# Kernel optimization log

Hardware: AMD Instinct MI355X
Metric: run time of the kernel (lower is better)

Reference implementation:

```python
import jax, jax.numpy as jnp
import numpy as np

N = 50000   # nodes
E = 800000  # edges
D = 256     # input feature dim
H = 128     # hidden size
OUT = 40    # output classes


def setup_inputs() -> dict:
    key = jax.random.key(0)
    ks = jax.random.split(key, 10)
    s = 0.05
    return {
        "x": jax.random.normal(ks[0], (N, D), jnp.float32),
        "edge_index": jax.random.randint(ks[1], (2, E), 0, N, dtype=jnp.int64),
        "W0": jax.random.normal(ks[2], (D, H), jnp.float32) * s,
        "b0": jnp.zeros((H,), jnp.float32),
        "W1": jax.random.normal(ks[3], (H, H), jnp.float32) * s,
        "b1": jnp.zeros((H,), jnp.float32),
        "W2": jax.random.normal(ks[4], (H, H), jnp.float32) * s,
        "b2": jnp.zeros((H,), jnp.float32),
        "Wout": jax.random.normal(ks[5], (H * 3, OUT), jnp.float32) * s,
        "bout": jnp.zeros((OUT,), jnp.float32),
    }


def _gcn_norm(edge_index, n):
    # PyG gcn_norm: add self-loops, symmetric D^-1/2 (A+I) D^-1/2 weights
    row, col = edge_index[0], edge_index[1]
    loop = jnp.arange(n, dtype=edge_index.dtype)
    row = jnp.concatenate([row, loop])
    col = jnp.concatenate([col, loop])
    deg = jax.ops.segment_sum(jnp.ones_like(col, jnp.float32), col, num_segments=n)
    dinv = jnp.where(deg > 0, jax.lax.rsqrt(jnp.maximum(deg, 1.0)), 0.0)
    norm = dinv[row] * dinv[col]  # [E+N]
    return row, col, norm


def _gcn_conv(x, W, b, row, col, norm, n):
    h = x @ W                                   # dense transform first (PyG order)
    msg = h[row] * norm[:, None]                # gather source feats, scale
    out = jax.ops.segment_sum(msg, col, num_segments=n)  # scatter-aggregate
    return out + b


def reference(x, edge_index, W0, b0, W1, b1, W2, b2, Wout, bout):
    n = x.shape[0]
    row, col, norm = _gcn_norm(edge_index, n)
    x1 = jax.nn.relu(_gcn_conv(x, W0, b0, row, col, norm, n))
    x2 = jax.nn.relu(_gcn_conv(x1, W1, b1, row, col, norm, n))
    x3 = jax.nn.relu(_gcn_conv(x2, W2, b2, row, col, norm, n))
    xs = jnp.concatenate([x1, x2, x3], axis=-1)  # JumpingKnowledge 'cat'
    return xs @ Wout + bout
```

## Files before the change

kernel.cpp:

```cpp
#include <hip/hip_runtime.h>

#define HID 128
#define NOUT 40
#define SCAN_B 256

typedef __attribute__((ext_vector_type(8))) short bf16x8;
typedef __attribute__((ext_vector_type(4))) float f32x4;

__device__ inline float bf2f(unsigned int u) {
    unsigned int t = u << 16;
    float f;
    __builtin_memcpy(&f, &t, 4);
    return f;
}
__device__ inline unsigned short f2bf(float f) {
    unsigned int x;
    __builtin_memcpy(&x, &f, 4);
    unsigned int r = (x + 0x7fffu + ((x >> 16) & 1u)) >> 16;
    return (unsigned short)r;
}
__device__ inline bf16x8 pack_bf8(float4 u, float4 v) {
    bf16x8 r;
    r[0] = (short)f2bf(u.x); r[1] = (short)f2bf(u.y);
    r[2] = (short)f2bf(u.z); r[3] = (short)f2bf(u.w);
    r[4] = (short)f2bf(v.x); r[5] = (short)f2bf(v.y);
    r[6] = (short)f2bf(v.z); r[7] = (short)f2bf(v.w);
    return r;
}

__global__ void detect_fmt_kernel(const unsigned int* __restrict__ e, int* __restrict__ flag) {
    int t = threadIdx.x;
    unsigned int v = e[2 * t + 1];
    unsigned long long ball = __ballot(v == 0u);
    if (t == 0) *flag = (ball == ~0ull) ? 1 : 0;
}

__global__ void degree_kernel(const void* __restrict__ eix, const int* __restrict__ flag,
                              int* __restrict__ deg, int E) {
    int i = blockIdx.x * blockDim.x + threadIdx.x;
    if (i >= E) return;
    int f = *flag;
    int c = f ? (int)(((const long long*)eix)[(size_t)E + i]) : ((const int*)eix)[(size_t)E + i];
    atomicAdd(&deg[c], 1);
}

__global__ void scan1_kernel(const int* __restrict__ deg, int* __restrict__ offs,
                             int* __restrict__ bsum, float* __restrict__ dinv, int N) {
    __shared__ int s[SCAN_B];
    int i = blockIdx.x * SCAN_B + threadIdx.x;
    int v = (i < N) ? deg[i] : 0;
    if (i < N) dinv[i] = rsqrtf((float)v + 1.0f);
    s[threadIdx.x] = v;
    __syncthreads();
    for (int d = 1; d < SCAN_B; d <<= 1) {
        int t = (threadIdx.x >= d) ? s[threadIdx.x - d] : 0;
        __syncthreads();
        s[threadIdx.x] += t;
        __syncthreads();
    }
    if (i < N) offs[i] = s[threadIdx.x] - v;
    if (threadIdx.x == SCAN_B - 1) bsum[blockIdx.x] = s[SCAN_B - 1];
}

__global__ void scan2_kernel(int* __restrict__ bsum, int nb) {
    __shared__ int s[SCAN_B];
    int v = (threadIdx.x < nb) ? bsum[threadIdx.x] : 0;
    s[threadIdx.x] = v;
    __syncthreads();
    for (int d = 1; d < SCAN_B; d <<= 1) {
        int t = (threadIdx.x >= d) ? s[threadIdx.x - d] : 0;
        __syncthreads();
        s[threadIdx.x] += t;
        __syncthreads();
    }
    if (threadIdx.x < nb) bsum[threadIdx.x] = s[threadIdx.x] - v;
}

__global__ void scan3_kernel(int* __restrict__ offs, const int* __restrict__ bsum,
                             int* __restrict__ cursor, int N, int E) {
    int i = blockIdx.x * SCAN_B + threadIdx.x;
    if (i < N) {
        int v = offs[i] + bsum[blockIdx.x];
        offs[i] = v;
        cursor[i] = v;
    }
    if (blockIdx.x == 0 && threadIdx.x == 0) offs[N] = E;
}

__global__ void fill_csr_kernel(const void* __restrict__ eix, const int* __restrict__ flag,
                                const float* __restrict__ dinv, int* __restrict__ cursor,
                                int2* __restrict__ pkd, int E) {
    int e = blockIdx.x * blockDim.x + threadIdx.x;
    if (e >= E) return;
    int f = *flag;
    int r, c;
    if (f) {
        r = (int)(((const long long*)eix)[e]);
        c = (int)(((const long long*)eix)[(size_t)E + e]);
    } else {
        r = ((const int*)eix)[e];
        c = ((const int*)eix)[(size_t)E + e];
    }
    int p = atomicAdd(&cursor[c], 1);
    float wv = dinv[r] * dinv[c];
    int2 rec;
    rec.x = r;
    rec.y = __float_as_int(wv);
    pkd[p] = rec;
}

__global__ void wt_all_kernel(const float* __restrict__ W0, const float* __restrict__ W1,
                              const float* __restrict__ W2, const float* __restrict__ Wo,
                              unsigned short* __restrict__ W0t, unsigned short* __restrict__ W1t,
                              unsigned short* __restrict__ W2t, unsigned short* __restrict__ Wot) {
    int idx = blockIdx.x * blockDim.x + threadIdx.x;
    const int s0 = 128 * 256, s1 = 128 * 128, s2 = 128 * 128, s3 = 48 * 384;
    if (idx < s0) {
        int n = idx >> 8, k = idx & 255;
        W0t[idx] = f2bf(W0[(size_t)k * 128 + n]);
    } else if ((idx -= s0) < s1) {
        int n = idx >> 7, k = idx & 127;
        W1t[idx] = f2bf(W1[(size_t)k * 128 + n]);
    } else if ((idx -= s1) < s2) {
        int n = idx >> 7, k = idx & 127;
        W2t[idx] = f2bf(W2[(size_t)k * 128 + n]);
    } else if ((idx -= s2) < s3) {
        int n = idx / 384, k = idx - n * 384;
        Wot[idx] = (n < NOUT) ? f2bf(Wo[(size_t)k * NOUT + n]) : (unsigned short)0;
    }
}

template <bool AF32>
__global__ __launch_bounds__(256) void gemm_mfma_kernel(
    const void* __restrict__ Ap, const unsigned short* __restrict__ Wt,
    unsigned short* __restrict__ H, int M, int K) {
    const int tid = threadIdx.x;
    const int lane = tid & 63;
    const int w = tid >> 6;
    const int wr = w >> 1, wc = w & 1;
    const int lr = lane & 15;
    const int ko = lane >> 4;
    const int bm = blockIdx.x * 64;

    f32x4 acc[2][4];
#pragma unroll
    for (int i = 0; i < 2; ++i)
#pragma unroll
        for (int j = 0; j < 4; ++j) acc[i][j] = (f32x4){0.f, 0.f, 0.f, 0.f};

    size_t aoff[2];
#pragma unroll
    for (int mi = 0; mi < 2; ++mi) {
        int R = bm + wr * 32 + mi * 16 + lr;
        if (R >= M) R = M - 1;
        aoff[mi] = (size_t)R * K + ko * 8;
    }
    size_t boff[4];
#pragma unroll
    for (int ni = 0; ni < 4; ++ni) {
        int n = wc * 64 + ni * 16 + lr;
        boff[ni] = (size_t)n * K + ko * 8;
    }

#pragma unroll 4
    for (int k0 = 0; k0 < K; k0 += 32) {
        bf16x8 a[2], b[4];
#pragma unroll
        for (int mi = 0; mi < 2; ++mi) {
            if constexpr (AF32) {
                const float* p = (const float*)Ap + aoff[mi] + k0;
                float4 u = *(const float4*)p;
                float4 v = *(const float4*)(p + 4);
                a[mi] = pack_bf8(u, v);
            } else {
                a[mi] = *(const bf16x8*)((const unsigned short*)Ap + aoff[mi] + k0);
            }
        }
#pragma unroll
        for (int ni = 0; ni < 4; ++ni) b[ni] = *(const bf16x8*)(Wt + boff[ni] + k0);
#pragma unroll
        for (int mi = 0; mi < 2; ++mi)
#pragma unroll
            for (int ni = 0; ni < 4; ++ni)
                acc[mi][ni] = __builtin_amdgcn_mfma_f32_16x16x32_bf16(a[mi], b[ni], acc[mi][ni], 0, 0, 0);
    }

#pragma unroll
    for (int mi = 0; mi < 2; ++mi) {
        int Rb = bm + wr * 32 + mi * 16 + ko * 4;
#pragma unroll
        for (int r = 0; r < 4; ++r) {
            int R = Rb + r;
            if (R < M) {
#pragma unroll
                for (int ni = 0; ni < 4; ++ni) {
                    int C = wc * 64 + ni * 16 + lr;
                    H[(size_t)R * HID + C] = f2bf(acc[mi][ni][r]);
                }
            }
        }
    }
}

__global__ __launch_bounds__(256) void agg_csr_kernel(
    const unsigned int* __restrict__ h32, const int* __restrict__ offs,
    const int2* __restrict__ pkd, const float* __restrict__ dinv,
    const float* __restrict__ bias, unsigned int* __restrict__ xo, int N) {
    const int lane = threadIdx.x & 63;
    const int n = (blockIdx.x * blockDim.x + threadIdx.x) >> 6;
    if (n >= N) return;
    const float d = dinv[n];
    unsigned int sv = h32[(size_t)n * 64 + lane];
    float ax = bf2f(sv & 0xffff) * (d * d) + bias[2 * lane + 0];
    float ay = bf2f(sv >> 16) * (d * d) + bias[2 * lane + 1];
    int e = offs[n];
    const int e1 = offs[n + 1];

    for (; e + 16 <= e1; e += 16) {
        int2 pk[16];
        unsigned int v[16];
#pragma unroll
        for (int j = 0; j < 16; ++j) pk[j] = pkd[e + j];
#pragma unroll
        for (int j = 0; j < 16; ++j) v[j] = h32[(size_t)pk[j].x * 64 + lane];
#pragma unroll
        for (int j = 0; j < 16; ++j) {
            float wv = __int_as_float(pk[j].y);
            ax += bf2f(v[j] & 0xffff) * wv;
            ay += bf2f(v[j] >> 16) * wv;
        }
    }
    for (; e + 4 <= e1; e += 4) {
        int2 pk[4];
        unsigned int v[4];
#pragma unroll
        for (int j = 0; j < 4; ++j) pk[j] = pkd[e + j];
#pragma unroll
        for (int j = 0; j < 4; ++j) v[j] = h32[(size_t)pk[j].x * 64 + lane];
#pragma unroll
        for (int j = 0; j < 4; ++j) {
            float wv = __int_as_float(pk[j].y);
            ax += bf2f(v[j] & 0xffff) * wv;
            ay += bf2f(v[j] >> 16) * wv;
        }
    }
    for (; e < e1; ++e) {
        int2 pk = pkd[e];
        unsigned int v = h32[(size_t)pk.x * 64 + lane];
        float wv = __int_as_float(pk.y);
        ax += bf2f(v & 0xffff) * wv;
        ay += bf2f(v >> 16) * wv;
    }
    ax = fmaxf(ax, 0.f);
    ay = fmaxf(ay, 0.f);
    xo[(size_t)n * 64 + lane] = (unsigned int)f2bf(ax) | ((unsigned int)f2bf(ay) << 16);
}

__global__ __launch_bounds__(256) void head_mfma_kernel(
    const unsigned short* __restrict__ x1, const unsigned short* __restrict__ x2,
    const unsigned short* __restrict__ x3, const unsigned short* __restrict__ Wt,
    const float* __restrict__ bout, float* __restrict__ out, int M) {
    const int tid = threadIdx.x;
    const int lane = tid & 63;
    const int w = tid >> 6;
    const int lr = lane & 15;
    const int ko = lane >> 4;
    const int bm = blockIdx.x * 64;
    int R = bm + w * 16 + lr;
    if (R >= M) R = M - 1;
    const unsigned short* xs[3] = {x1, x2, x3};

    f32x4 acc[3];
#pragma unroll
    for (int i = 0; i < 3; ++i) acc[i] = (f32x4){0.f, 0.f, 0.f, 0.f};

#pragma unroll
    for (int s = 0; s < 3; ++s) {
        const unsigned short* xp = xs[s] + (size_t)R * HID + ko * 8;
#pragma unroll
        for (int c = 0; c < 4; ++c) {
            bf16x8 a = *(const bf16x8*)(xp + c * 32);
#pragma unroll
            for (int ni = 0; ni < 3; ++ni) {
                bf16x8 b = *(const bf16x8*)(Wt + (size_t)(ni * 16 + lr) * 384 + s * 128 + c * 32 + ko * 8);
                acc[ni] = __builtin_amdgcn_mfma_f32_16x16x32_bf16(a, b, acc[ni], 0, 0, 0);
            }
        }
    }

    int Rb = bm + w * 16 + ko * 4;
#pragma unroll
    for (int r = 0; r < 4; ++r) {
        int Ro = Rb + r;
        if (Ro < M) {
#pragma unroll
            for (int ni = 0; ni < 3; ++ni) {
                int C = ni * 16 + lr;
                if (C < NOUT) out[(size_t)Ro * NOUT + C] = acc[ni][r] + bout[C];
            }
        }
    }
}

static inline size_t align_up(size_t x, size_t a) { return (x + a - 1) / a * a; }

extern "C" void kernel_launch(void* const* d_in, const int* in_sizes, int n_in,
                              void* d_out, int out_size, void* d_ws, size_t ws_size,
                              hipStream_t stream) {
    const float* x    = (const float*)d_in[0];
    const void*  eix  = d_in[1];
    const float* W0   = (const float*)d_in[2];
    const float* b0   = (const float*)d_in[3];
    const float* W1   = (const float*)d_in[4];
    const float* b1   = (const float*)d_in[5];
    const float* W2   = (const float*)d_in[6];
    const float* b2   = (const float*)d_in[7];
    const float* Wout = (const float*)d_in[8];
    const float* bout = (const float*)d_in[9];
    float* out = (float*)d_out;

    const int D = 256;
    const int N = in_sizes[0] / D;
    const int E = in_sizes[1] / 2;

    char* w = (char*)d_ws;
    size_t off = 0;
    int* deg = (int*)(w + off);             off = align_up(off + (size_t)N * 4, 256);
    float* dinv = (float*)(w + off);        off = align_up(off + (size_t)N * 4, 256);
    int* offs = (int*)(w + off);            off = align_up(off + (size_t)(N + 1) * 4, 256);
    int* cursor = (int*)(w + off);          off = align_up(off + (size_t)N * 4, 256);
    int* bsum = (int*)(w + off);            off = align_up(off + 1024 * 4, 256);
    int* flag = (int*)(w + off);            off = align_up(off + 16, 256);
    int2* pkd = (int2*)(w + off);           off = align_up(off + (size_t)E * 8, 256);
    unsigned short* h   = (unsigned short*)(w + off); off = align_up(off + (size_t)N * HID * 2, 256);
    unsigned short* x1b = (unsigned short*)(w + off); off = align_up(off + (size_t)N * HID * 2, 256);
    unsigned short* x2b = (unsigned short*)(w + off); off = align_up(off + (size_t)N * HID * 2, 256);
    unsigned short* x3b = (unsigned short*)(w + off); off = align_up(off + (size_t)N * HID * 2, 256);
    unsigned short* W0t = (unsigned short*)(w + off); off = align_up(off + (size_t)HID * 256 * 2, 256);
    unsigned short* W1t = (unsigned short*)(w + off); off = align_up(off + (size_t)HID * HID * 2, 256);
    unsigned short* W2t = (unsigned short*)(w + off); off = align_up(off + (size_t)HID * HID * 2, 256);
    unsigned short* Wot = (unsigned short*)(w + off); off = align_up(off + (size_t)48 * 384 * 2, 256);
    (void)ws_size;

    detect_fmt_kernel<<<1, 64, 0, stream>>>((const unsigned int*)eix, flag);
    hipMemsetAsync(deg, 0, (size_t)N * 4, stream);
    degree_kernel<<<(E + 255) / 256, 256, 0, stream>>>(eix, flag, deg, E);

    const int nb = (N + SCAN_B - 1) / SCAN_B;
    scan1_kernel<<<nb, SCAN_B, 0, stream>>>(deg, offs, bsum, dinv, N);
    scan2_kernel<<<1, SCAN_B, 0, stream>>>(bsum, nb);
    scan3_kernel<<<nb, SCAN_B, 0, stream>>>(offs, bsum, cursor, N, E);
    fill_csr_kernel<<<(E + 255) / 256, 256, 0, stream>>>(eix, flag, dinv, cursor, pkd, E);

    const int wtTot = 128 * 256 + 128 * 128 + 128 * 128 + 48 * 384;
    wt_all_kernel<<<(wtTot + 255) / 256, 256, 0, stream>>>(W0, W1, W2, Wout, W0t, W1t, W2t, Wot);

    const int gGemm = (N + 63) / 64;
    const int gAgg = (N * 64 + 255) / 256;

    gemm_mfma_kernel<true><<<gGemm, 256, 0, stream>>>(x, W0t, h, N, 256);
    agg_csr_kernel<<<gAgg, 256, 0, stream>>>((const unsigned int*)h, offs, pkd, dinv, b0, (unsigned int*)x1b, N);
    gemm_mfma_kernel<false><<<gGemm, 256, 0, stream>>>(x1b, W1t, h, N, HID);
    agg_csr_kernel<<<gAgg, 256, 0, stream>>>((const unsigned int*)h, offs, pkd, dinv, b1, (unsigned int*)x2b, N);
    gemm_mfma_kernel<false><<<gGemm, 256, 0, stream>>>(x2b, W2t, h, N, HID);
    agg_csr_kernel<<<gAgg, 256, 0, stream>>>((const unsigned int*)h, offs, pkd, dinv, b2, (unsigned int*)x3b, N);
    head_mfma_kernel<<<gGemm, 256, 0, stream>>>(x1b, x2b, x3b, Wot, bout, out, N);
}
```

Measured before the change: 390.4 us.

## Store CSR as source indices only and bucket fill atomics by destination window

The CSR fill kernel now stages a chunk of edges in shared memory and runs its scatter atomics in 16 destination-node windows, so writes into the CSR array land in more local regions. The per-edge normalisation weight is no longer stored. Each edge record shrinks from int2 to int, and the aggregation kernel recomputes the weight as dinv[src]*dinv[dst]. This halves index traffic in the three aggregation passes and the fill writes, at the cost of one extra dinv gather per edge and 16 sequential passes over shared memory in the fill kernel.

```diff
diff --git a/kernel.cpp b/kernel.cpp
--- a/kernel.cpp
+++ b/kernel.cpp
@@ -3,6 +3,8 @@
 #define HID 128
 #define NOUT 40
 #define SCAN_B 256
+#define CHUNK 4096
+#define NWIN 16
 
 typedef __attribute__((ext_vector_type(8))) short bf16x8;
 typedef __attribute__((ext_vector_type(4))) float f32x4;
@@ -87,26 +89,41 @@
     if (blockIdx.x == 0 && threadIdx.x == 0) offs[N] = E;
 }
 
-__global__ void fill_csr_kernel(const void* __restrict__ eix, const int* __restrict__ flag,
-                                const float* __restrict__ dinv, int* __restrict__ cursor,
-                                int2* __restrict__ pkd, int E) {
-    int e = blockIdx.x * blockDim.x + threadIdx.x;
-    if (e >= E) return;
-    int f = *flag;
-    int r, c;
-    if (f) {
-        r = (int)(((const long long*)eix)[e]);
-        c = (int)(((const long long*)eix)[(size_t)E + e]);
-    } else {
-        r = ((const int*)eix)[e];
-        c = ((const int*)eix)[(size_t)E + e];
-    }
-    int p = atomicAdd(&cursor[c], 1);
-    float wv = dinv[r] * dinv[c];
-    int2 rec;
-    rec.x = r;
-    rec.y = __float_as_int(wv);
-    pkd[p] = rec;
+__global__ __launch_bounds__(256) void fill_csr_kernel(
+    const void* __restrict__ eix, const int* __restrict__ flag,
+    int* __restrict__ cursor, int* __restrict__ csrc, int E, int N) {
+    __shared__ int lr[CHUNK];
+    __shared__ int lc[CHUNK];
+    const int e0 = blockIdx.x * CHUNK;
+    const int cnt = min(CHUNK, E - e0);
+    const int f = *flag;
+    for (int i = threadIdx.x; i < cnt; i += 256) {
+        int r, c;
+        if (f) {
+            r = (int)(((const long long*)eix)[e0 + i]);
+            c = (int)(((const long long*)eix)[(size_t)E + e0 + i]);
+        } else {
+            r = ((const int*)eix)[e0 + i];
+            c = ((const int*)eix)[(size_t)E + e0 + i];
+        }
+        lr[i] = r;
+        lc[i] = c;
+    }
+    __syncthreads();
+    const int wsz = (N + NWIN - 1) / NWIN;
+#pragma unroll 1
+    for (int wn = 0; wn < NWIN; ++wn) {
+        const int lo = wn * wsz;
+        const int hi = lo + wsz;
+        for (int i = threadIdx.x; i < cnt; i += 256) {
+            int c = lc[i];
+            if (c >= lo && c < hi) {
+                int p = atomicAdd(&cursor[c], 1);
+                csrc[p] = lr[i];
+            }
+        }
+        __syncthreads();
+    }
 }
 
 __global__ void wt_all_kernel(const float* __restrict__ W0, const float* __restrict__ W1,
@@ -204,7 +221,7 @@
 
 __global__ __launch_bounds__(256) void agg_csr_kernel(
     const unsigned int* __restrict__ h32, const int* __restrict__ offs,
-    const int2* __restrict__ pkd, const float* __restrict__ dinv,
+    const int* __restrict__ csrc, const float* __restrict__ dinv,
     const float* __restrict__ bias, unsigned int* __restrict__ xo, int N) {
     const int lane = threadIdx.x & 63;
     const int n = (blockIdx.x * blockDim.x + threadIdx.x) >> 6;
@@ -217,39 +234,45 @@
     const int e1 = offs[n + 1];
 
     for (; e + 16 <= e1; e += 16) {
-        int2 pk[16];
+        int r[16];
         unsigned int v[16];
-#pragma unroll
-        for (int j = 0; j < 16; ++j) pk[j] = pkd[e + j];
-#pragma unroll
-        for (int j = 0; j < 16; ++j) v[j] = h32[(size_t)pk[j].x * 64 + lane];
+        float wv[16];
+#pragma unroll
+        for (int j = 0; j < 16; ++j) r[j] = csrc[e + j];
+#pragma unroll
+        for (int j = 0; j < 16; ++j) v[j] = h32[(size_t)r[j] * 64 + lane];
+#pragma unroll
+        for (int j = 0; j < 16; ++j) wv[j] = dinv[r[j]];
 #pragma unroll
         for (int j = 0; j < 16; ++j) {
-            float wv = __int_as_float(pk[j].y);
-            ax += bf2f(v[j] & 0xffff) * wv;
-            ay += bf2f(v[j] >> 16) * wv;
+            float wd = wv[j] * d;
+            ax += bf2f(v[j] & 0xffff) * wd;
+            ay += bf2f(v[j] >> 16) * wd;
         }
     }
     for (; e + 4 <= e1; e += 4) {
-        int2 pk[4];
+        int r[4];
         unsigned int v[4];
-#pragma unroll
-        for (int j = 0; j < 4; ++j) pk[j] = pkd[e + j];
-#pragma unroll
-        for (int j = 0; j < 4; ++j) v[j] = h32[(size_t)pk[j].x * 64 + lane];
+        float wv[4];
+#pragma unroll
+        for (int j = 0; j < 4; ++j) r[j] = csrc[e + j];
+#pragma unroll
+        for (int j = 0; j < 4; ++j) v[j] = h32[(size_t)r[j] * 64 + lane];
+#pragma unroll
+        for (int j = 0; j < 4; ++j) wv[j] = dinv[r[j]];
 #pragma unroll
         for (int j = 0; j < 4; ++j) {
-            float wv = __int_as_float(pk[j].y);
-            ax += bf2f(v[j] & 0xffff) * wv;
-            ay += bf2f(v[j] >> 16) * wv;
+            float wd = wv[j] * d;
+            ax += bf2f(v[j] & 0xffff) * wd;
+            ay += bf2f(v[j] >> 16) * wd;
         }
     }
     for (; e < e1; ++e) {
-        int2 pk = pkd[e];
-        unsigned int v = h32[(size_t)pk.x * 64 + lane];
-        float wv = __int_as_float(pk.y);
-        ax += bf2f(v & 0xffff) * wv;
-        ay += bf2f(v >> 16) * wv;
+        int r = csrc[e];
+        unsigned int v = h32[(size_t)r * 64 + lane];
+        float wd = dinv[r] * d;
+        ax += bf2f(v & 0xffff) * wd;
+        ay += bf2f(v >> 16) * wd;
     }
     ax = fmaxf(ax, 0.f);
     ay = fmaxf(ay, 0.f);
@@ -331,7 +354,7 @@
     int* cursor = (int*)(w + off);          off = align_up(off + (size_t)N * 4, 256);
     int* bsum = (int*)(w + off);            off = align_up(off + 1024 * 4, 256);
     int* flag = (int*)(w + off);            off = align_up(off + 16, 256);
-    int2* pkd = (int2*)(w + off);           off = align_up(off + (size_t)E * 8, 256);
+    int* csrc = (int*)(w + off);            off = align_up(off + (size_t)E * 4, 256);
     unsigned short* h   = (unsigned short*)(w + off); off = align_up(off + (size_t)N * HID * 2, 256);
     unsigned short* x1b = (unsigned short*)(w + off); off = align_up(off + (size_t)N * HID * 2, 256);
     unsigned short* x2b = (unsigned short*)(w + off); off = align_up(off + (size_t)N * HID * 2, 256);
@@ -350,7 +373,7 @@
     scan1_kernel<<<nb, SCAN_B, 0, stream>>>(deg, offs, bsum, dinv, N);
     scan2_kernel<<<1, SCAN_B, 0, stream>>>(bsum, nb);
     scan3_kernel<<<nb, SCAN_B, 0, stream>>>(offs, bsum, cursor, N, E);
-    fill_csr_kernel<<<(E + 255) / 256, 256, 0, stream>>>(eix, flag, dinv, cursor, pkd, E);
+    fill_csr_kernel<<<(E + CHUNK - 1) / CHUNK, 256, 0, stream>>>(eix, flag, cursor, csrc, E, N);
 
     const int wtTot = 128 * 256 + 128 * 128 + 128 * 128 + 48 * 384;
     wt_all_kernel<<<(wtTot + 255) / 256, 256, 0, stream>>>(W0, W1, W2, Wout, W0t, W1t, W2t, Wot);
@@ -359,10 +382,10 @@
     const int gAgg = (N * 64 + 255) / 256;
 
     gemm_mfma_kernel<true><<<gGemm, 256, 0, stream>>>(x, W0t, h, N, 256);
-    agg_csr_kernel<<<gAgg, 256, 0, stream>>>((const unsigned int*)h, offs, pkd, dinv, b0, (unsigned int*)x1b, N);
+    agg_csr_kernel<<<gAgg, 256, 0, stream>>>((const unsigned int*)h, offs, csrc, dinv, b0, (unsigned int*)x1b, N);
     gemm_mfma_kernel<false><<<gGemm, 256, 0, stream>>>(x1b, W1t, h, N, HID);
-    agg_csr_kernel<<<gAgg, 256, 0, stream>>>((const unsigned int*)h, offs, pkd, dinv, b1, (unsigned int*)x2b, N);
+    agg_csr_kernel<<<gAgg, 256, 0, stream>>>((const unsigned int*)h, offs, csrc, dinv, b1, (unsigned int*)x2b, N);
     gemm_mfma_kernel<false><<<gGemm, 256, 0, stream>>>(x2b, W2t, h, N, HID);
-    agg_csr_kernel<<<gAgg, 256, 0, stream>>>((const unsigned int*)h, offs, pkd, dinv, b2, (unsigned int*)x3b, N);
+    agg_csr_kernel<<<gAgg, 256, 0, stream>>>((const unsigned int*)h, offs, csrc, dinv, b2, (unsigned int*)x3b, N);
     head_mfma_kernel<<<gGemm, 256, 0, stream>>>(x1b, x2b, x3b, Wot, bout, out, N);
 }
```

Result: slower. 458.9 us (+17.6%).

## Window CSR fill by destination range and give GEMM waves full-width row tiles

Applied to the files above, without the earlier changes.

The CSR fill kernel now runs as a grid-stride loop. Each block handles only edges whose destination falls in one of 8 node windows, so the atomic cursor updates and the scattered pkd writes stay within a smaller address range and should get better cache locality. The cost is that every edge index is read 8 times. Separately, the GEMM now gives each wave 16 rows by all 128 columns instead of 32x64, which trades A-operand reuse for loading more of the B matrix per wave.

```diff
diff --git a/kernel.cpp b/kernel.cpp
--- a/kernel.cpp
+++ b/kernel.cpp
@@ -3,6 +3,7 @@
 #define HID 128
 #define NOUT 40
 #define SCAN_B 256
+#define NWIN 8
 
 typedef __attribute__((ext_vector_type(8))) short bf16x8;
 typedef __attribute__((ext_vector_type(4))) float f32x4;
@@ -87,26 +88,34 @@
     if (blockIdx.x == 0 && threadIdx.x == 0) offs[N] = E;
 }
 
-__global__ void fill_csr_kernel(const void* __restrict__ eix, const int* __restrict__ flag,
-                                const float* __restrict__ dinv, int* __restrict__ cursor,
-                                int2* __restrict__ pkd, int E) {
-    int e = blockIdx.x * blockDim.x + threadIdx.x;
-    if (e >= E) return;
-    int f = *flag;
-    int r, c;
-    if (f) {
-        r = (int)(((const long long*)eix)[e]);
-        c = (int)(((const long long*)eix)[(size_t)E + e]);
-    } else {
-        r = ((const int*)eix)[e];
-        c = ((const int*)eix)[(size_t)E + e];
-    }
-    int p = atomicAdd(&cursor[c], 1);
-    float wv = dinv[r] * dinv[c];
-    int2 rec;
-    rec.x = r;
-    rec.y = __float_as_int(wv);
-    pkd[p] = rec;
+__global__ __launch_bounds__(256) void fill_csr_kernel(
+    const void* __restrict__ eix, const int* __restrict__ flag,
+    const float* __restrict__ dinv, int* __restrict__ cursor,
+    int2* __restrict__ pkd, int E, int N) {
+    const int wn = blockIdx.x & (NWIN - 1);
+    const int slice = blockIdx.x >> 3;
+    const int nslice = gridDim.x >> 3;
+    const int wsz = (N + NWIN - 1) / NWIN;
+    const int lo = wn * wsz, hi = lo + wsz;
+    const int f = *flag;
+    const int stride = nslice * 256;
+    for (int i = slice * 256 + threadIdx.x; i < E; i += stride) {
+        int r, c;
+        if (f) {
+            r = (int)(((const long long*)eix)[i]);
+            c = (int)(((const long long*)eix)[(size_t)E + i]);
+        } else {
+            r = ((const int*)eix)[i];
+            c = ((const int*)eix)[(size_t)E + i];
+        }
+        if (c >= lo && c < hi) {
+            int p = atomicAdd(&cursor[c], 1);
+            int2 rec;
+            rec.x = r;
+            rec.y = __float_as_int(dinv[r] * dinv[c]);
+            pkd[p] = rec;
+        }
+    }
 }
 
 __global__ void wt_all_kernel(const float* __restrict__ W0, const float* __restrict__ W1,
@@ -137,66 +146,48 @@
     const int tid = threadIdx.x;
     const int lane = tid & 63;
     const int w = tid >> 6;
-    const int wr = w >> 1, wc = w & 1;
     const int lr = lane & 15;
     const int ko = lane >> 4;
     const int bm = blockIdx.x * 64;
 
-    f32x4 acc[2][4];
-#pragma unroll
-    for (int i = 0; i < 2; ++i)
-#pragma unroll
-        for (int j = 0; j < 4; ++j) acc[i][j] = (f32x4){0.f, 0.f, 0.f, 0.f};
-
-    size_t aoff[2];
-#pragma unroll
-    for (int mi = 0; mi < 2; ++mi) {
-        int R = bm + wr * 32 + mi * 16 + lr;
-        if (R >= M) R = M - 1;
-        aoff[mi] = (size_t)R * K + ko * 8;
-    }
-    size_t boff[4];
-#pragma unroll
-    for (int ni = 0; ni < 4; ++ni) {
-        int n = wc * 64 + ni * 16 + lr;
-        boff[ni] = (size_t)n * K + ko * 8;
-    }
+    f32x4 acc[8];
+#pragma unroll
+    for (int j = 0; j < 8; ++j) acc[j] = (f32x4){0.f, 0.f, 0.f, 0.f};
+
+    int R = bm + w * 16 + lr;
+    if (R >= M) R = M - 1;
+    const size_t aoff = (size_t)R * K + ko * 8;
+    size_t boff[8];
+#pragma unroll
+    for (int ni = 0; ni < 8; ++ni) boff[ni] = (size_t)(ni * 16 + lr) * K + ko * 8;
 
 #pragma unroll 4
     for (int k0 = 0; k0 < K; k0 += 32) {
-        bf16x8 a[2], b[4];
-#pragma unroll
-        for (int mi = 0; mi < 2; ++mi) {
-            if constexpr (AF32) {
-                const float* p = (const float*)Ap + aoff[mi] + k0;
-                float4 u = *(const float4*)p;
-                float4 v = *(const float4*)(p + 4);
-                a[mi] = pack_bf8(u, v);
-            } else {
-                a[mi] = *(const bf16x8*)((const unsigned short*)Ap + aoff[mi] + k0);
-            }
-        }
-#pragma unroll
-        for (int ni = 0; ni < 4; ++ni) b[ni] = *(const bf16x8*)(Wt + boff[ni] + k0);
-#pragma unroll
-        for (int mi = 0; mi < 2; ++mi)
-#pragma unroll
-            for (int ni = 0; ni < 4; ++ni)
-                acc[mi][ni] = __builtin_amdgcn_mfma_f32_16x16x32_bf16(a[mi], b[ni], acc[mi][ni], 0, 0, 0);
-    }
-
-#pragma unroll
-    for (int mi = 0; mi < 2; ++mi) {
-        int Rb = bm + wr * 32 + mi * 16 + ko * 4;
-#pragma unroll
-        for (int r = 0; r < 4; ++r) {
-            int R = Rb + r;
-            if (R < M) {
-#pragma unroll
-                for (int ni = 0; ni < 4; ++ni) {
-                    int C = wc * 64 + ni * 16 + lr;
-                    H[(size_t)R * HID + C] = f2bf(acc[mi][ni][r]);
-                }
+        bf16x8 a, b[8];
+        if constexpr (AF32) {
+            const float* p = (const float*)Ap + aoff + k0;
+            float4 u = *(const float4*)p;
+            float4 v = *(const float4*)(p + 4);
+            a = pack_bf8(u, v);
+        } else {
+            a = *(const bf16x8*)((const unsigned short*)Ap + aoff + k0);
+        }
+#pragma unroll
+        for (int ni = 0; ni < 8; ++ni) b[ni] = *(const bf16x8*)(Wt + boff[ni] + k0);
+#pragma unroll
+        for (int ni = 0; ni < 8; ++ni)
+            acc[ni] = __builtin_amdgcn_mfma_f32_16x16x32_bf16(a, b[ni], acc[ni], 0, 0, 0);
+    }
+
+    const int Rb = bm + w * 16 + ko * 4;
+#pragma unroll
+    for (int r = 0; r < 4; ++r) {
+        int Ro = Rb + r;
+        if (Ro < M) {
+#pragma unroll
+            for (int ni = 0; ni < 8; ++ni) {
+                int C = ni * 16 + lr;
+                H[(size_t)Ro * HID + C] = f2bf(acc[ni][r]);
             }
         }
     }
@@ -350,7 +341,7 @@
     scan1_kernel<<<nb, SCAN_B, 0, stream>>>(deg, offs, bsum, dinv, N);
     scan2_kernel<<<1, SCAN_B, 0, stream>>>(bsum, nb);
     scan3_kernel<<<nb, SCAN_B, 0, stream>>>(offs, bsum, cursor, N, E);
-    fill_csr_kernel<<<(E + 255) / 256, 256, 0, stream>>>(eix, flag, dinv, cursor, pkd, E);
+    fill_csr_kernel<<<NWIN * 256, 256, 0, stream>>>(eix, flag, dinv, cursor, pkd, E, N);
 
     const int wtTot = 128 * 256 + 128 * 128 + 128 * 128 + 48 * 384;
     wt_all_kernel<<<(wtTot + 255) / 256, 256, 0, stream>>>(W0, W1, W2, Wout, W0t, W1t, W2t, Wot);
```

Result: slower. 404.2 us (+3.5%).
